# Optimization experiments

Measured on AMD Instinct MI355X. Metric: run time of the kernel, lower is better.

## Reference

```python
import jax, jax.numpy as jnp
import numpy as np

N_TOKEN = 8192
N_EMBED = 256

def setup_inputs() -> dict:
    key = jax.random.key(0)
    k1, k2 = jax.random.split(key)
    inputs = jax.random.normal(k1, (8, 2048, N_EMBED), dtype=jnp.float32)
    embeds = jax.random.normal(k2, (N_TOKEN, N_EMBED), dtype=jnp.float32)
    return {"inputs": inputs, "embeds": embeds}

def reference(inputs, embeds):
    size = inputs.shape
    x = inputs.reshape(-1, N_EMBED)                      # [N, D]
    dists = (
        jnp.sum(x * x, axis=-1, keepdims=True)
        + jnp.sum(embeds * embeds, axis=-1)[None, :]
        - 2.0 * jnp.matmul(x, embeds.T)
    )
    indices = jnp.argmin(dists, axis=-1)                 # [N]
    quantized_embs = embeds[indices]                     # gather [N, D]
    # straight-through estimator
    quantized = x + jax.lax.stop_gradient(quantized_embs - x)
    return quantized.reshape(size)
```

## Files before the change

### kernel.cpp

```cpp
#include <hip/hip_runtime.h>
#include <hip/hip_fp16.h>
#include <cstdint>
#include <cfloat>
#include <cstddef>

#define N_TOK 16384
#define K_CODE 8192
#define D_EMB 256
#define BM 128
#define BN 128
#define KSPLIT 8
#define KRANGE (K_CODE / KSPLIT)
#define NCAND (KSPLIT * 3)

typedef __attribute__((ext_vector_type(4))) int   i32x4;
typedef __attribute__((ext_vector_type(4))) float f32x4;

__device__ __forceinline__ unsigned umin_(unsigned a, unsigned b) { return a < b ? a : b; }
__device__ __forceinline__ unsigned umax_(unsigned a, unsigned b) { return a > b ? a : b; }
__device__ __forceinline__ unsigned med3_(unsigned a, unsigned b, unsigned c) {
  unsigned d;
  asm("v_med3_u32 %0, %1, %2, %3" : "=v"(d) : "v"(a), "v"(b), "v"(c));
  return d;
}
__device__ __forceinline__ unsigned enc_f32(float v) {
  unsigned u = __float_as_uint(v);
  return (u & 0x80000000u) ? ~u : (u | 0x80000000u);
}
__device__ __forceinline__ int q8(float x) {
  return __float2int_rn(fminf(fmaxf(x * 16.0f, -127.0f), 127.0f));
}
__device__ __forceinline__ int q8n(float x) {
  return __float2int_rn(fminf(fmaxf(x * -16.0f, -127.0f), 127.0f));
}

__global__ __launch_bounds__(256) void prep_kernel(
    const float* __restrict__ inputs, const float* __restrict__ embeds,
    int* __restrict__ Aq, int* __restrict__ Bq,
    float* __restrict__ e2f, unsigned* __restrict__ e2s) {
  const int nb_e = K_CODE / 4;
  if (blockIdx.x < nb_e) {
    const int row  = blockIdx.x * 4 + (threadIdx.x >> 6);
    const int lane = threadIdx.x & 63;
    const float4 v = *reinterpret_cast<const float4*>(embeds + (size_t)row * D_EMB + lane * 4);
    float s = v.x * v.x + v.y * v.y + v.z * v.z + v.w * v.w;
#pragma unroll
    for (int m = 32; m > 0; m >>= 1) s += __shfl_xor(s, m, 64);
    if (lane == 0) {
      e2f[row] = s;
      e2s[row] = ((unsigned)__float2int_rn(s * 256.0f)) << 13;
    }
    const int p = (q8(v.x) & 255) | ((q8(v.y) & 255) << 8) |
                  ((q8(v.z) & 255) << 16) | (q8(v.w) << 24);
    Bq[row * 64 + lane] = p;
  } else {
    const int j = (blockIdx.x - nb_e) * 256 + threadIdx.x;
    const float4 v = *reinterpret_cast<const float4*>(inputs + (size_t)j * 4);
    const int p = (q8n(v.x) & 255) | ((q8n(v.y) & 255) << 8) |
                  ((q8n(v.z) & 255) << 16) | (q8n(v.w) << 24);
    Aq[j] = p;
  }
}

__global__ __launch_bounds__(256, 2) void vq_mfma_kernel(
    const char* __restrict__ Aq,
    const char* __restrict__ Bq,
    const unsigned* __restrict__ e2s,
    unsigned* __restrict__ cand_out) {
  __shared__ char Bsmem[2][BN * D_EMB];
  __shared__ unsigned candL[2][BM][3];

  const int tid  = threadIdx.x;
  const int lane = tid & 63;
  const int wid  = tid >> 6;
  const int wr   = wid >> 1;
  const int wc   = wid & 1;
  const int lrow = lane & 15;
  const int lk   = lane >> 4;

  const int mtile = blockIdx.x & 127;
  const int kpart = blockIdx.x >> 7;
  const int m0    = mtile * BM;
  const int kbeg  = kpart * KRANGE;

  int srow[8], scol[8], ldsb[8];
#pragma unroll
  for (int i = 0; i < 8; ++i) {
    const int h  = i >> 2;
    const int bb = (i & 3) * 4096 + tid * 16;
    const int r  = bb >> 7;
    const int s  = (bb >> 4) & 7;
    srow[i] = r;
    scol[i] = h * 128 + (s ^ (r & 7)) * 16;
    ldsb[i] = h * 16384 + bb;
  }

#pragma unroll
  for (int i = 0; i < 8; ++i) {
    __builtin_amdgcn_global_load_lds(
        (const __attribute__((address_space(1))) void*)(
            Aq + (size_t)(m0 + srow[i]) * D_EMB + scol[i]),
        (__attribute__((address_space(3))) void*)(&Bsmem[1][0] + ldsb[i]), 16, 0, 0);
  }
#pragma unroll
  for (int i = 0; i < 8; ++i) {
    __builtin_amdgcn_global_load_lds(
        (const __attribute__((address_space(1))) void*)(
            Bq + (size_t)(kbeg + srow[i]) * D_EMB + scol[i]),
        (__attribute__((address_space(3))) void*)(&Bsmem[0][0] + ldsb[i]), 16, 0, 0);
  }
  __syncthreads();

  i32x4 afrag[4][4];
#pragma unroll
  for (int mi = 0; mi < 4; ++mi)
#pragma unroll
    for (int ks = 0; ks < 4; ++ks) {
      const int hbase = (ks >> 1) * 16384;
      const int kbyte = (ks & 1) * 64 + lk * 16;
      const int row = wr * 64 + mi * 16 + lrow;
      const int off = hbase + row * 128 + (kbyte ^ ((row & 7) << 4));
      afrag[mi][ks] = *reinterpret_cast<const i32x4*>(&Bsmem[1][0] + off);
    }
  __syncthreads();

  unsigned t1[4][4], t2[4][4], t3[4][4];
#pragma unroll
  for (int mi = 0; mi < 4; ++mi)
#pragma unroll
    for (int r = 0; r < 4; ++r) {
      t1[mi][r] = 0xFFFFFFFFu; t2[mi][r] = 0xFFFFFFFFu; t3[mi][r] = 0xFFFFFFFFu;
    }

  for (int kt = 0; kt < KRANGE / BN; ++kt) {
    const int k0 = kbeg + kt * BN;
    const char* Bb = &Bsmem[kt & 1][0];

    if (kt + 1 < KRANGE / BN) {
      const int kn = kbeg + (kt + 1) * BN;
      char* Bn = &Bsmem[(kt + 1) & 1][0];
#pragma unroll
      for (int i = 0; i < 8; ++i) {
        __builtin_amdgcn_global_load_lds(
            (const __attribute__((address_space(1))) void*)(
                Bq + (size_t)(kn + srow[i]) * D_EMB + scol[i]),
            (__attribute__((address_space(3))) void*)(Bn + ldsb[i]), 16, 0, 0);
      }
    }

    i32x4 acc[4][4];
#pragma unroll
    for (int mi = 0; mi < 4; ++mi)
#pragma unroll
      for (int ni = 0; ni < 4; ++ni) acc[mi][ni] = (i32x4)0;

#pragma unroll
    for (int ks = 0; ks < 4; ++ks) {
      const int hbase = (ks >> 1) * 16384;
      const int kbyte = (ks & 1) * 64 + lk * 16;
      i32x4 bfr[4];
#pragma unroll
      for (int ni = 0; ni < 4; ++ni) {
        const int row = wc * 64 + ni * 16 + lrow;
        const int off = hbase + row * 128 + (kbyte ^ ((row & 7) << 4));
        bfr[ni] = *reinterpret_cast<const i32x4*>(Bb + off);
      }
#pragma unroll
      for (int mi = 0; mi < 4; ++mi)
#pragma unroll
        for (int ni = 0; ni < 4; ++ni)
          acc[mi][ni] = __builtin_amdgcn_mfma_i32_16x16x64_i8(
              afrag[mi][ks], bfr[ni], acc[mi][ni], 0, 0, 0);
    }

    const int colb = k0 + wc * 64;
    unsigned E4[4];
#pragma unroll
    for (int ni = 0; ni < 4; ++ni) {
      const int col = colb + ni * 16 + lrow;
      E4[ni] = e2s[col] | (unsigned)col;
    }
#pragma unroll
    for (int mi = 0; mi < 4; ++mi)
#pragma unroll
      for (int r = 0; r < 4; ++r) {
#pragma unroll
        for (int ni = 0; ni < 4; ++ni) {
          const unsigned p = (((unsigned)acc[mi][ni][r]) << 14) + E4[ni];
          const unsigned o1 = t1[mi][r], o2 = t2[mi][r];
          t1[mi][r] = umin_(o1, p);
          t2[mi][r] = med3_(o1, o2, p);
          t3[mi][r] = med3_(o2, t3[mi][r], p);
        }
      }

    __syncthreads();
  }

#pragma unroll
  for (int mi = 0; mi < 4; ++mi)
#pragma unroll
    for (int r = 0; r < 4; ++r) {
      unsigned a1 = t1[mi][r], a2 = t2[mi][r], a3 = t3[mi][r];
#pragma unroll
      for (int m = 1; m <= 8; m <<= 1) {
        const unsigned b1 = (unsigned)__shfl_xor((int)a1, m, 64);
        const unsigned b2 = (unsigned)__shfl_xor((int)a2, m, 64);
        const unsigned b3 = (unsigned)__shfl_xor((int)a3, m, 64);
        unsigned l1 = umax_(a1, b1); a1 = umin_(a1, b1);
        unsigned l2 = umax_(a2, l1); a2 = umin_(a2, l1);
        a3 = umin_(a3, l2);
        l1 = umax_(a1, b2); a1 = umin_(a1, b2);
        l2 = umax_(a2, l1); a2 = umin_(a2, l1);
        a3 = umin_(a3, l2);
        a3 = umin_(a3, b3);
      }
      if (lrow == 0) {
        const int row = wr * 64 + mi * 16 + lk * 4 + r;
        candL[wc][row][0] = a1;
        candL[wc][row][1] = a2;
        candL[wc][row][2] = a3;
      }
    }
  __syncthreads();
  if (tid < BM) {
    unsigned a1 = candL[0][tid][0], a2 = candL[0][tid][1], a3 = candL[0][tid][2];
    const unsigned b1 = candL[1][tid][0], b2 = candL[1][tid][1], b3 = candL[1][tid][2];
    unsigned l1 = umax_(a1, b1); a1 = umin_(a1, b1);
    unsigned l2 = umax_(a2, l1); a2 = umin_(a2, l1);
    a3 = umin_(a3, l2);
    l1 = umax_(a1, b2); a1 = umin_(a1, b2);
    l2 = umax_(a2, l1); a2 = umin_(a2, l1);
    a3 = umin_(a3, l2);
    a3 = umin_(a3, b3);
    cand_out[(size_t)(kpart * 3 + 0) * N_TOK + m0 + tid] = a1;
    cand_out[(size_t)(kpart * 3 + 1) * N_TOK + m0 + tid] = a2;
    cand_out[(size_t)(kpart * 3 + 2) * N_TOK + m0 + tid] = a3;
  }
}

__global__ __launch_bounds__(256) void refine24_kernel(
    const float* __restrict__ inputs, const float* __restrict__ embeds,
    const float* __restrict__ e2, const unsigned* __restrict__ cand,
    float* __restrict__ out) {
  const int token = blockIdx.x * 4 + (threadIdx.x >> 6);
  const int lane  = threadIdx.x & 63;

  unsigned v = 0xFFFFFFFFu;
  if (lane < NCAND) v = cand[(size_t)lane * N_TOK + token];
  int picks[6];
#pragma unroll
  for (int rnd = 0; rnd < 6; ++rnd) {
    unsigned m = v;
#pragma unroll
    for (int s = 32; s > 0; s >>= 1) m = umin_(m, (unsigned)__shfl_xor((int)m, s, 64));
    picks[rnd] = (int)(m & 0x1FFFu);
    if (v == m) v = 0xFFFFFFFFu;
  }

  const float4 xv = *reinterpret_cast<const float4*>(inputs + (size_t)token * D_EMB + lane * 4);
  float dots[6];
#pragma unroll
  for (int c = 0; c < 6; ++c) {
    const float4 ev = *reinterpret_cast<const float4*>(embeds + (size_t)picks[c] * D_EMB + lane * 4);
    float d = xv.x * ev.x;
    d = fmaf(xv.y, ev.y, d); d = fmaf(xv.z, ev.z, d); d = fmaf(xv.w, ev.w, d);
    dots[c] = d;
  }
#pragma unroll
  for (int c = 0; c < 6; ++c)
#pragma unroll
    for (int m = 32; m > 0; m >>= 1) dots[c] += __shfl_xor(dots[c], m, 64);

  unsigned long long best = ~0ull;
#pragma unroll
  for (int c = 0; c < 6; ++c) {
    const float dist = fmaf(-2.0f, dots[c], e2[picks[c]]);
    const unsigned long long p =
        ((unsigned long long)enc_f32(dist) << 32) | (unsigned)picks[c];
    if (p < best) best = p;
  }
  const int widx = (int)(best & 0xFFFFFFFFull);
  const float4 ov = *reinterpret_cast<const float4*>(embeds + (size_t)widx * D_EMB + lane * 4);
  *reinterpret_cast<float4*>(out + (size_t)token * D_EMB + lane * 4) = ov;
}

__global__ __launch_bounds__(256) void e2_kernel(const float* __restrict__ embeds,
                                                 float* __restrict__ e2) {
  const int row  = blockIdx.x * 4 + (threadIdx.x >> 6);
  const int lane = threadIdx.x & 63;
  float4 v = *reinterpret_cast<const float4*>(embeds + (size_t)row * D_EMB + lane * 4);
  float s = v.x * v.x + v.y * v.y + v.z * v.z + v.w * v.w;
#pragma unroll
  for (int m = 32; m > 0; m >>= 1) s += __shfl_xor(s, m, 64);
  if (lane == 0) e2[row] = s;
}

__global__ __launch_bounds__(256, 2) void vq_score_kernel(
    const float* __restrict__ inputs, const float* __restrict__ embeds,
    const float* __restrict__ e2, unsigned long long* __restrict__ keys) {
  __shared__ float A_lds[32 * 132];
  __shared__ float B_lds[32 * 132];
  const int tid = threadIdx.x;
  const int tx = tid & 15, ty = tid >> 4;
  const int mtile = blockIdx.x & 127, kpart = blockIdx.x >> 7;
  const int m0 = mtile * BM, kbeg = kpart * KRANGE;
  float best[8]; int bidx[8];
#pragma unroll
  for (int i = 0; i < 8; ++i) { best[i] = FLT_MAX; bidx[i] = 0x7FFFFFFF; }
  for (int k0 = kbeg; k0 < kbeg + KRANGE; k0 += 128) {
    float acc[8][8];
#pragma unroll
    for (int i = 0; i < 8; ++i)
#pragma unroll
      for (int j = 0; j < 8; ++j) acc[i][j] = 0.0f;
    for (int d0 = 0; d0 < D_EMB; d0 += 32) {
      __syncthreads();
#pragma unroll
      for (int it = 0; it < 4; ++it) {
        const int u = tid + it * 256, m = u >> 3, dg = u & 7;
        float4 va = *reinterpret_cast<const float4*>(inputs + (size_t)(m0 + m) * D_EMB + d0 + dg * 4);
        float4 vb = *reinterpret_cast<const float4*>(embeds + (size_t)(k0 + m) * D_EMB + d0 + dg * 4);
        A_lds[(dg * 4 + 0) * 132 + m] = va.x; A_lds[(dg * 4 + 1) * 132 + m] = va.y;
        A_lds[(dg * 4 + 2) * 132 + m] = va.z; A_lds[(dg * 4 + 3) * 132 + m] = va.w;
        B_lds[(dg * 4 + 0) * 132 + m] = vb.x; B_lds[(dg * 4 + 1) * 132 + m] = vb.y;
        B_lds[(dg * 4 + 2) * 132 + m] = vb.z; B_lds[(dg * 4 + 3) * 132 + m] = vb.w;
      }
      __syncthreads();
#pragma unroll 8
      for (int dd = 0; dd < 32; ++dd) {
        float a[8], b[8];
        *reinterpret_cast<float4*>(&a[0]) = *reinterpret_cast<const float4*>(&A_lds[dd * 132 + ty * 8]);
        *reinterpret_cast<float4*>(&a[4]) = *reinterpret_cast<const float4*>(&A_lds[dd * 132 + ty * 8 + 4]);
        *reinterpret_cast<float4*>(&b[0]) = *reinterpret_cast<const float4*>(&B_lds[dd * 132 + tx * 8]);
        *reinterpret_cast<float4*>(&b[4]) = *reinterpret_cast<const float4*>(&B_lds[dd * 132 + tx * 8 + 4]);
#pragma unroll
        for (int i = 0; i < 8; ++i)
#pragma unroll
          for (int j = 0; j < 8; ++j) acc[i][j] = fmaf(a[i], b[j], acc[i][j]);
      }
    }
#pragma unroll
    for (int j = 0; j < 8; ++j) {
      const int col = k0 + tx * 8 + j;
      const float ev = e2[col];
#pragma unroll
      for (int i = 0; i < 8; ++i) {
        const float dist = fmaf(-2.0f, acc[i][j], ev);
        if (dist < best[i]) { best[i] = dist; bidx[i] = col; }
      }
    }
  }
  __syncthreads();
  float* bestv = A_lds;
  int* besti = reinterpret_cast<int*>(B_lds);
#pragma unroll
  for (int i = 0; i < 8; ++i) {
    bestv[(ty * 8 + i) * 16 + tx] = best[i];
    besti[(ty * 8 + i) * 16 + tx] = bidx[i];
  }
  __syncthreads();
  if (tid < BM) {
    float bv = FLT_MAX; int bi = 0x7FFFFFFF;
#pragma unroll
    for (int t = 0; t < 16; ++t) {
      const float v = bestv[tid * 16 + t];
      const int ii = besti[tid * 16 + t];
      if (v < bv || (v == bv && ii < bi)) { bv = v; bi = ii; }
    }
    keys[(size_t)kpart * N_TOK + m0 + tid] =
        ((unsigned long long)enc_f32(bv) << 32) | (unsigned)bi;
  }
}

__global__ __launch_bounds__(256) void gather_kernel(
    const float* __restrict__ embeds, const unsigned long long* __restrict__ keys,
    float* __restrict__ out) {
  const int r    = blockIdx.x * 4 + (threadIdx.x >> 6);
  const int lane = threadIdx.x & 63;
  unsigned long long k = keys[r];
#pragma unroll
  for (int p = 1; p < KSPLIT; ++p) {
    const unsigned long long kp = keys[(size_t)p * N_TOK + r];
    if (kp < k) k = kp;
  }
  const int idx = (int)(k & 0xFFFFFFFFull);
  float4 v = *reinterpret_cast<const float4*>(embeds + (size_t)idx * D_EMB + lane * 4);
  *reinterpret_cast<float4*>(out + (size_t)r * D_EMB + lane * 4) = v;
}

extern "C" void kernel_launch(void* const* d_in, const int* in_sizes, int n_in,
                              void* d_out, int out_size, void* d_ws, size_t ws_size,
                              hipStream_t stream) {
  const float* inputs = (const float*)d_in[0];
  const float* embeds = (const float*)d_in[1];
  float* out = (float*)d_out;

  char* ws = (char*)d_ws;
  float*    e2f = (float*)ws;
  unsigned* e2s = (unsigned*)(ws + 65536);
  unsigned* cand = (unsigned*)(ws + (1 << 20));
  unsigned long long* keys = (unsigned long long*)(ws + (1 << 20));
  char* Aq = ws + (4 << 20);
  char* Bq = ws + (8 << 20);
  const size_t need = (size_t)(10 << 20);

  if (ws_size >= need) {
    const int nb = K_CODE / 4 + (N_TOK * D_EMB / 4) / 256;
    prep_kernel<<<nb, 256, 0, stream>>>(inputs, embeds, (int*)Aq, (int*)Bq, e2f, e2s);
    vq_mfma_kernel<<<(N_TOK / BM) * KSPLIT, 256, 0, stream>>>(Aq, Bq, e2s, cand);
    refine24_kernel<<<N_TOK / 4, 256, 0, stream>>>(inputs, embeds, e2f, cand, out);
  } else {
    e2_kernel<<<K_CODE / 4, 256, 0, stream>>>(embeds, e2f);
    vq_score_kernel<<<(N_TOK / BM) * KSPLIT, 256, 0, stream>>>(inputs, embeds, e2f, keys);
    gather_kernel<<<N_TOK / 4, 256, 0, stream>>>(embeds, keys, out);
  }
}
```

Baseline: 75.90 us.

## Shrink codebook tile to 64 and give each wave its own 32 rows

Halves the codebook tile (BN 128→64), so each wave now covers 32 token rows across all 64 codes instead of a 64x64 quadrant. This removes the cross-wave candidate merge through shared memory and its extra barrier, and lets each wave write its top-3 candidates straight to global memory. Smaller per-wave accumulator and top-3 state, plus half the LDS, aims to fit three blocks per CU instead of two. In exchange every wave reloads the full B tile each step, which doubles LDS reads per MFMA, and the loop runs twice as many iterations, each with its own barrier.

Result: faster. 69.45 us (-8.5%).

```diff
diff --git a/kernel.cpp b/kernel.cpp
--- a/kernel.cpp
+++ b/kernel.cpp
@@ -8,9 +8,10 @@
 #define K_CODE 8192
 #define D_EMB 256
 #define BM 128
-#define BN 128
+#define BN 64
 #define KSPLIT 8
 #define KRANGE (K_CODE / KSPLIT)
+#define NTILE (KRANGE / BN)
 #define NCAND (KSPLIT * 3)
 
 typedef __attribute__((ext_vector_type(4))) int   i32x4;
@@ -62,19 +63,16 @@
   }
 }
 
-__global__ __launch_bounds__(256, 2) void vq_mfma_kernel(
+__global__ __launch_bounds__(256, 3) void vq_mfma_kernel(
     const char* __restrict__ Aq,
     const char* __restrict__ Bq,
     const unsigned* __restrict__ e2s,
     unsigned* __restrict__ cand_out) {
   __shared__ char Bsmem[2][BN * D_EMB];
-  __shared__ unsigned candL[2][BM][3];
 
   const int tid  = threadIdx.x;
   const int lane = tid & 63;
   const int wid  = tid >> 6;
-  const int wr   = wid >> 1;
-  const int wc   = wid & 1;
   const int lrow = lane & 15;
   const int lk   = lane >> 4;
 
@@ -83,27 +81,48 @@
   const int m0    = mtile * BM;
   const int kbeg  = kpart * KRANGE;
 
-  int srow[8], scol[8], ldsb[8];
-#pragma unroll
-  for (int i = 0; i < 8; ++i) {
-    const int h  = i >> 2;
-    const int bb = (i & 3) * 4096 + tid * 16;
+  int srow[4], scol[4], ldsb[4];
+#pragma unroll
+  for (int i = 0; i < 4; ++i) {
+    const int h  = i >> 1;
+    const int bb = (i & 1) * 4096 + tid * 16;
     const int r  = bb >> 7;
     const int s  = (bb >> 4) & 7;
     srow[i] = r;
     scol[i] = h * 128 + (s ^ (r & 7)) * 16;
-    ldsb[i] = h * 16384 + bb;
-  }
-
-#pragma unroll
-  for (int i = 0; i < 8; ++i) {
+    ldsb[i] = h * 8192 + bb;
+  }
+
+#pragma unroll
+  for (int i = 0; i < 4; ++i) {
     __builtin_amdgcn_global_load_lds(
         (const __attribute__((address_space(1))) void*)(
             Aq + (size_t)(m0 + srow[i]) * D_EMB + scol[i]),
+        (__attribute__((address_space(3))) void*)(&Bsmem[0][0] + ldsb[i]), 16, 0, 0);
+    __builtin_amdgcn_global_load_lds(
+        (const __attribute__((address_space(1))) void*)(
+            Aq + (size_t)(m0 + 64 + srow[i]) * D_EMB + scol[i]),
         (__attribute__((address_space(3))) void*)(&Bsmem[1][0] + ldsb[i]), 16, 0, 0);
   }
-#pragma unroll
-  for (int i = 0; i < 8; ++i) {
+  __syncthreads();
+
+  i32x4 afrag[2][4];
+  {
+    const char* Ab = &Bsmem[wid >> 1][0];
+#pragma unroll
+    for (int mi = 0; mi < 2; ++mi)
+#pragma unroll
+      for (int ks = 0; ks < 4; ++ks) {
+        const int row = (wid & 1) * 32 + mi * 16 + lrow;
+        const int off = (ks >> 1) * 8192 + row * 128 +
+                        (((ks & 1) * 64 + lk * 16) ^ ((row & 7) << 4));
+        afrag[mi][ks] = *reinterpret_cast<const i32x4*>(Ab + off);
+      }
+  }
+  __syncthreads();
+
+#pragma unroll
+  for (int i = 0; i < 4; ++i) {
     __builtin_amdgcn_global_load_lds(
         (const __attribute__((address_space(1))) void*)(
             Bq + (size_t)(kbeg + srow[i]) * D_EMB + scol[i]),
@@ -111,36 +130,23 @@
   }
   __syncthreads();
 
-  i32x4 afrag[4][4];
-#pragma unroll
-  for (int mi = 0; mi < 4; ++mi)
-#pragma unroll
-    for (int ks = 0; ks < 4; ++ks) {
-      const int hbase = (ks >> 1) * 16384;
-      const int kbyte = (ks & 1) * 64 + lk * 16;
-      const int row = wr * 64 + mi * 16 + lrow;
-      const int off = hbase + row * 128 + (kbyte ^ ((row & 7) << 4));
-      afrag[mi][ks] = *reinterpret_cast<const i32x4*>(&Bsmem[1][0] + off);
-    }
-  __syncthreads();
-
-  unsigned t1[4][4], t2[4][4], t3[4][4];
-#pragma unroll
-  for (int mi = 0; mi < 4; ++mi)
+  unsigned t1[2][4], t2[2][4], t3[2][4];
+#pragma unroll
+  for (int mi = 0; mi < 2; ++mi)
 #pragma unroll
     for (int r = 0; r < 4; ++r) {
       t1[mi][r] = 0xFFFFFFFFu; t2[mi][r] = 0xFFFFFFFFu; t3[mi][r] = 0xFFFFFFFFu;
     }
 
-  for (int kt = 0; kt < KRANGE / BN; ++kt) {
+  for (int kt = 0; kt < NTILE; ++kt) {
     const int k0 = kbeg + kt * BN;
     const char* Bb = &Bsmem[kt & 1][0];
 
-    if (kt + 1 < KRANGE / BN) {
+    if (kt + 1 < NTILE) {
       const int kn = kbeg + (kt + 1) * BN;
       char* Bn = &Bsmem[(kt + 1) & 1][0];
 #pragma unroll
-      for (int i = 0; i < 8; ++i) {
+      for (int i = 0; i < 4; ++i) {
         __builtin_amdgcn_global_load_lds(
             (const __attribute__((address_space(1))) void*)(
                 Bq + (size_t)(kn + srow[i]) * D_EMB + scol[i]),
@@ -148,40 +154,39 @@
       }
     }
 
-    i32x4 acc[4][4];
-#pragma unroll
-    for (int mi = 0; mi < 4; ++mi)
+    i32x4 acc[2][4];
+#pragma unroll
+    for (int mi = 0; mi < 2; ++mi)
 #pragma unroll
       for (int ni = 0; ni < 4; ++ni) acc[mi][ni] = (i32x4)0;
 
 #pragma unroll
     for (int ks = 0; ks < 4; ++ks) {
-      const int hbase = (ks >> 1) * 16384;
+      const int hbase = (ks >> 1) * 8192;
       const int kbyte = (ks & 1) * 64 + lk * 16;
       i32x4 bfr[4];
 #pragma unroll
       for (int ni = 0; ni < 4; ++ni) {
-        const int row = wc * 64 + ni * 16 + lrow;
+        const int row = ni * 16 + lrow;
         const int off = hbase + row * 128 + (kbyte ^ ((row & 7) << 4));
         bfr[ni] = *reinterpret_cast<const i32x4*>(Bb + off);
       }
 #pragma unroll
-      for (int mi = 0; mi < 4; ++mi)
+      for (int mi = 0; mi < 2; ++mi)
 #pragma unroll
         for (int ni = 0; ni < 4; ++ni)
           acc[mi][ni] = __builtin_amdgcn_mfma_i32_16x16x64_i8(
               afrag[mi][ks], bfr[ni], acc[mi][ni], 0, 0, 0);
     }
 
-    const int colb = k0 + wc * 64;
     unsigned E4[4];
 #pragma unroll
     for (int ni = 0; ni < 4; ++ni) {
-      const int col = colb + ni * 16 + lrow;
+      const int col = k0 + ni * 16 + lrow;
       E4[ni] = e2s[col] | (unsigned)col;
     }
 #pragma unroll
-    for (int mi = 0; mi < 4; ++mi)
+    for (int mi = 0; mi < 2; ++mi)
 #pragma unroll
       for (int r = 0; r < 4; ++r) {
 #pragma unroll
@@ -198,7 +203,7 @@
   }
 
 #pragma unroll
-  for (int mi = 0; mi < 4; ++mi)
+  for (int mi = 0; mi < 2; ++mi)
 #pragma unroll
     for (int r = 0; r < 4; ++r) {
       unsigned a1 = t1[mi][r], a2 = t2[mi][r], a3 = t3[mi][r];
@@ -216,27 +221,12 @@
         a3 = umin_(a3, b3);
       }
       if (lrow == 0) {
-        const int row = wr * 64 + mi * 16 + lk * 4 + r;
-        candL[wc][row][0] = a1;
-        candL[wc][row][1] = a2;
-        candL[wc][row][2] = a3;
-      }
-    }
-  __syncthreads();
-  if (tid < BM) {
-    unsigned a1 = candL[0][tid][0], a2 = candL[0][tid][1], a3 = candL[0][tid][2];
-    const unsigned b1 = candL[1][tid][0], b2 = candL[1][tid][1], b3 = candL[1][tid][2];
-    unsigned l1 = umax_(a1, b1); a1 = umin_(a1, b1);
-    unsigned l2 = umax_(a2, l1); a2 = umin_(a2, l1);
-    a3 = umin_(a3, l2);
-    l1 = umax_(a1, b2); a1 = umin_(a1, b2);
-    l2 = umax_(a2, l1); a2 = umin_(a2, l1);
-    a3 = umin_(a3, l2);
-    a3 = umin_(a3, b3);
-    cand_out[(size_t)(kpart * 3 + 0) * N_TOK + m0 + tid] = a1;
-    cand_out[(size_t)(kpart * 3 + 1) * N_TOK + m0 + tid] = a2;
-    cand_out[(size_t)(kpart * 3 + 2) * N_TOK + m0 + tid] = a3;
-  }
+        const int grow = m0 + wid * 32 + mi * 16 + lk * 4 + r;
+        cand_out[(size_t)(kpart * 3 + 0) * N_TOK + grow] = a1;
+        cand_out[(size_t)(kpart * 3 + 1) * N_TOK + grow] = a2;
+        cand_out[(size_t)(kpart * 3 + 2) * N_TOK + grow] = a3;
+      }
+    }
 }
 
 __global__ __launch_bounds__(256) void refine24_kernel(
```
